# Optimization experiments

Measured on AMD Instinct MI355X. Metric: run time of the kernel, lower is better.

The kernel has to match this reference:

```python
import jax, jax.numpy as jnp
import numpy as np

N_NET, D, N_H, N_T, N_IN, N_OUT = 1, 4, 8, 2048, 256, 256


def setup_inputs() -> dict:
    key = jax.random.key(0)
    k1, k2, k3 = jax.random.split(key, 3)
    r_prime = jax.random.normal(k1, (N_NET, D, N_T, N_IN), dtype=jnp.float32)
    # learned params per __init__: E ~ N(0, 0.02), Q ~ N(0, 0.02)
    E = 0.02 * jax.random.normal(k2, (N_NET, N_H, N_OUT, N_IN), dtype=jnp.float32)
    Q = 0.02 * jax.random.normal(k3, (N_NET, N_H, N_IN, N_IN), dtype=jnp.float32)
    return {"r_prime": r_prime, "E": E, "Q": Q}


def reference(r_prime, E, Q):
    n_t = r_prime.shape[2]
    # Omega[N,b,h,t,u] = r'[N,b,t,i] Q[N,h,i,j] r'[N,b,u,j]  (bilinear scores, no softmax)
    Omega = jnp.einsum('Nbti,Nhij,Nbuj->Nbhtu', r_prime, Q, r_prime)
    mask = jnp.tril(jnp.ones((n_t, n_t), dtype=Omega.dtype))  # causal lower-triangular
    Omega = Omega * mask
    # r[N,b,t,i] = Omega[N,b,h,t,u] E[N,h,i,j] r'[N,b,u,j]
    r = jnp.einsum('Nbhtu,Nhij,Nbuj->Nbti', Omega, E, r_prime)
    return r
```

## Files before the change

kernel.cpp:

```cpp
#include <hip/hip_runtime.h>
#include <stdint.h>

typedef unsigned short u16;
typedef __attribute__((ext_vector_type(4))) float f32x4;
typedef __attribute__((ext_vector_type(4))) uint32_t u32x4;
typedef __attribute__((ext_vector_type(8))) __bf16 bf16x8;

#define B_ 4
#define H_ 8
#define T_ 2048
#define C_ 256
#define KC 2048
#define NCH 32
#define XP 528
#define SP 144

static __device__ __forceinline__ f32x4 mfma16(u32x4 a, u32x4 b, f32x4 c) {
  union { u32x4 u; bf16x8 b; } A, Bb;
  A.u = a; Bb.u = b;
  return __builtin_amdgcn_mfma_f32_16x16x32_bf16(A.b, Bb.b, c, 0, 0, 0);
}
static __device__ __forceinline__ u16 f2b(float f) {
  union { __bf16 h; u16 u; } r; r.h = (__bf16)f; return r.u;
}

__global__ __launch_bounds__(256) void k_prep(const float* __restrict__ rp_f,
                                              const float* __restrict__ E_f,
                                              const float* __restrict__ Q_f,
                                              u16* __restrict__ rbf,
                                              u16* __restrict__ rpT,
                                              u16* __restrict__ qtb,
                                              u16* __restrict__ ec) {
  __shared__ u16 l[64][72];
  const int r = blockIdx.x, tid = threadIdx.x;
  if (r < 512) {
    const int b = r >> 7, i0 = ((r >> 5) & 3) * 64, t0 = (r & 31) * 64;
    const int tj = tid & 63, tq = tid >> 6;
    const float* src = rp_f + (size_t)b * T_ * C_;
    u16* rb = rbf + (size_t)b * T_ * C_;
    #pragma unroll
    for (int rr = 0; rr < 16; ++rr) {
      int tl = rr * 4 + tq;
      u16 v = f2b(src[(size_t)(t0 + tl) * C_ + i0 + tj]);
      l[tl][tj] = v;
      rb[(size_t)(t0 + tl) * C_ + i0 + tj] = v;
    }
    __syncthreads();
    u16* dst = rpT + (size_t)b * C_ * T_;
    #pragma unroll
    for (int rr = 0; rr < 16; ++rr) {
      int il = rr * 4 + tq;
      dst[(size_t)(i0 + il) * T_ + t0 + tj] = l[tj][il];
    }
  } else if (r < 640) {
    const int q = r - 512;
    const int h = q >> 4, i0 = ((q >> 2) & 3) * 64, j0 = (q & 3) * 64;
    const int tj = tid & 63, tq = tid >> 6;
    const float* qh = Q_f + (size_t)h * C_ * C_;
    #pragma unroll
    for (int rr = 0; rr < 16; ++rr) {
      int i = rr * 4 + tq;
      l[i][tj] = f2b(qh[(size_t)(i0 + i) * C_ + j0 + tj]);
    }
    __syncthreads();
    u16* qth = qtb + (size_t)h * C_ * C_;
    #pragma unroll
    for (int rr = 0; rr < 16; ++rr) {
      int j = rr * 4 + tq;
      qth[(size_t)(j0 + j) * C_ + i0 + tj] = l[tj][j];
    }
  } else {
    const int q = r - 640;
    size_t e = ((size_t)q * 256 + tid) * 4;
    int h = (int)(e >> 16), i = (int)((e >> 8) & 255), j = (int)(e & 255);
    f32x4 v = *(const f32x4*)(E_f + e);
    union { u16 h4[4]; uint64_t qq; } p;
    #pragma unroll
    for (int c = 0; c < 4; ++c) p.h4[c] = f2b(v[c]);
    *(uint64_t*)(ec + (size_t)i * KC + h * 256 + j) = p.qq;
  }
}

__global__ __launch_bounds__(256) void k_gram(const u16* __restrict__ rpT,
                                              u16* __restrict__ G) {
  __shared__ u16 gls[4][16][20];
  const int js = blockIdx.x, iq = blockIdx.y, b = blockIdx.z;
  const int tid = threadIdx.x, lane = tid & 63, v = tid >> 6;
  const int l15 = lane & 15, lq = lane >> 4;
  const u16* rtb = rpT + (size_t)b * C_ * T_;
  const int irow = 64 * iq + 16 * v;
  const int rrow = lane >> 2, rc4 = (lane & 3) * 4;

  f32x4 acc = (f32x4)0.f;

  for (int k = 0; k < NCH; ++k) {
    #pragma unroll
    for (int rr = 0; rr < 4; ++rr)
      gls[v][4 * lq + rr][l15] = f2b(acc[rr]);
    __builtin_amdgcn_wave_barrier();
    u16* gk = G + (size_t)(b * NCH + k) * C_ * C_;
    *(uint64_t*)(gk + (size_t)(irow + rrow) * C_ + 16 * js + rc4) =
        *(const uint64_t*)&gls[v][rrow][rc4];
    __builtin_amdgcn_wave_barrier();

    u32x4 am[2], bn[2];
    #pragma unroll
    for (int kk = 0; kk < 2; ++kk) {
      am[kk] = *(const u32x4*)(rtb + (size_t)(irow + l15) * T_ +
                               64 * k + 32 * kk + 8 * lq);
      bn[kk] = *(const u32x4*)(rtb + (size_t)(16 * js + l15) * T_ +
                               64 * k + 32 * kk + 8 * lq);
    }
    #pragma unroll
    for (int kk = 0; kk < 2; ++kk)
      acc = mfma16(am[kk], bn[kk], acc);
  }
}

__global__ __launch_bounds__(256, 2) void k_z(const u16* __restrict__ rbf,
                                              const u16* __restrict__ rpT,
                                              const u16* __restrict__ qtb,
                                              const u16* __restrict__ G,
                                              u16* __restrict__ ZC) {
  __shared__ __align__(16) char rp_l[64 * XP];
  __shared__ __align__(16) char x_l[64 * XP];
  __shared__ __align__(16) char s_l[64 * SP];

  const int tile = blockIdx.x, b = blockIdx.y, h = blockIdx.z;
  const int t0 = tile * 64;
  const int tid = threadIdx.x, lane = tid & 63, v = tid >> 6;
  const int l15 = lane & 15, lq = lane >> 4;

  const u16* rpb = rbf + (size_t)b * T_ * C_;
  const u16* rtb = rpT + (size_t)b * C_ * T_;
  const u16* gt  = G + (size_t)(b * NCH + tile) * C_ * C_;
  const u16* qth = qtb + (size_t)h * C_ * C_;

  {
    const int row = tid >> 2, seg = tid & 3;
    const char* src = (const char*)(rpb + (size_t)(t0 + row) * C_);
    #pragma unroll
    for (int c = 0; c < 8; ++c) {
      u32x4 vv = *(const u32x4*)(src + seg * 128 + c * 16);
      *(u32x4*)(rp_l + (size_t)row * XP + seg * 128 + c * 16) = vv;
    }
  }
  __syncthreads();

  #pragma unroll
  for (int mh = 0; mh < 2; ++mh) {
    u32x4 am[2][8];
    #pragma unroll
    for (int mq = 0; mq < 2; ++mq)
      #pragma unroll
      for (int kk = 0; kk < 8; ++kk)
        am[mq][kk] = *(const u32x4*)(rp_l +
            (size_t)(32 * mh + 16 * mq + l15) * XP + 64 * kk + 16 * lq);
    #pragma unroll
    for (int n = 0; n < 4; ++n) {
      f32x4 qacc[2];
      qacc[0] = (f32x4)0.f; qacc[1] = (f32x4)0.f;
      #pragma unroll
      for (int kk = 0; kk < 8; ++kk) {
        u32x4 bq = *(const u32x4*)(qth +
            (size_t)(64 * v + 16 * n + l15) * C_ + 32 * kk + 8 * lq);
        qacc[0] = mfma16(am[0][kk], bq, qacc[0]);
        qacc[1] = mfma16(am[1][kk], bq, qacc[1]);
      }
      #pragma unroll
      for (int mq = 0; mq < 2; ++mq)
        #pragma unroll
        for (int rr = 0; rr < 4; ++rr)
          *(u16*)(x_l + (size_t)(32 * mh + 16 * mq + 4 * lq + rr) * XP +
                  (64 * v + 16 * n + l15) * 2) = f2b(qacc[mq][rr]);
    }
  }
  __syncthreads();

  f32x4 acc[4][4];
  #pragma unroll
  for (int m = 0; m < 4; ++m)
    #pragma unroll
    for (int n = 0; n < 4; ++n) acc[m][n] = (f32x4)0.f;

  #pragma unroll
  for (int n = 0; n < 4; ++n) {
    u32x4 bg[8];
    #pragma unroll
    for (int kk = 0; kk < 8; ++kk)
      bg[kk] = *(const u32x4*)(gt +
          (size_t)(64 * v + 16 * n + l15) * C_ + 32 * kk + 8 * lq);
    #pragma unroll
    for (int mm = 0; mm < 4; ++mm) {
      u32x4 qa2[8];
      #pragma unroll
      for (int kk = 0; kk < 8; ++kk)
        qa2[kk] = *(const u32x4*)(x_l + (size_t)(16 * mm + l15) * XP +
                                  64 * kk + 16 * lq);
      #pragma unroll
      for (int kk = 0; kk < 8; ++kk)
        acc[mm][n] = mfma16(qa2[kk], bg[kk], acc[mm][n]);
    }
  }

  {
    f32x4 sacc[4];
    #pragma unroll
    for (int m = 0; m < 4; ++m) sacc[m] = (f32x4)0.f;
    u32x4 bs[8];
    #pragma unroll
    for (int kk = 0; kk < 8; ++kk)
      bs[kk] = *(const u32x4*)(rp_l + (size_t)(16 * v + l15) * XP +
                               64 * kk + 16 * lq);
    #pragma unroll
    for (int mm = 0; mm < 4; ++mm) {
      u32x4 qa2[8];
      #pragma unroll
      for (int kk = 0; kk < 8; ++kk)
        qa2[kk] = *(const u32x4*)(x_l + (size_t)(16 * mm + l15) * XP +
                                  64 * kk + 16 * lq);
      #pragma unroll
      for (int kk = 0; kk < 8; ++kk)
        sacc[mm] = mfma16(qa2[kk], bs[kk], sacc[mm]);
    }
    #pragma unroll
    for (int m = 0; m < 4; ++m)
      #pragma unroll
      for (int rr = 0; rr < 4; ++rr) {
        int tl = 16 * m + 4 * lq + rr;
        int ul = 16 * v + l15;
        float sv = (ul > tl) ? 0.f : sacc[m][rr];
        *(u16*)(s_l + (size_t)tl * SP + ul * 2) = f2b(sv);
      }
  }
  __syncthreads();

  {
    u32x4 sa[4][2];
    #pragma unroll
    for (int m = 0; m < 4; ++m)
      #pragma unroll
      for (int kk = 0; kk < 2; ++kk)
        sa[m][kk] = *(const u32x4*)(s_l + (size_t)(16 * m + l15) * SP +
                                    64 * kk + 16 * lq);
    #pragma unroll
    for (int n = 0; n < 4; ++n)
      #pragma unroll
      for (int kk = 0; kk < 2; ++kk) {
        u32x4 vb = *(const u32x4*)(rtb +
            (size_t)(64 * v + 16 * n + l15) * T_ + t0 + 32 * kk + 8 * lq);
        #pragma unroll
        for (int m = 0; m < 4; ++m)
          acc[m][n] = mfma16(sa[m][kk], vb, acc[m][n]);
      }
  }

  #pragma unroll
  for (int m = 0; m < 4; ++m)
    #pragma unroll
    for (int n = 0; n < 4; ++n)
      #pragma unroll
      for (int rr = 0; rr < 4; ++rr)
        *(u16*)(x_l + (size_t)(16 * m + 4 * lq + rr) * XP +
                (64 * v + 16 * n + l15) * 2) = f2b(acc[m][n][rr]);
  __syncthreads();
  {
    const int row = tid >> 2, seg = tid & 3;
    char* dst = (char*)(ZC + ((size_t)(b * T_ + t0 + row) * KC + h * 256));
    #pragma unroll
    for (int c = 0; c < 8; ++c) {
      u32x4 vv = *(const u32x4*)(x_l + (size_t)row * XP + seg * 128 + c * 16);
      *(u32x4*)(dst + seg * 128 + c * 16) = vv;
    }
  }
}

__global__ __launch_bounds__(256) void k_o(const u16* __restrict__ ZC,
                                           const u16* __restrict__ ec,
                                           float* __restrict__ out) {
  const int mt = blockIdx.x, b = blockIdx.y;
  const int tid = threadIdx.x, lane = tid & 63, v = tid >> 6;
  const int l15 = lane & 15, lq = lane >> 4;

  const u16* za_b = ZC + (size_t)(b * T_ + mt * 32) * KC;

  f32x4 acc[2][4];
  #pragma unroll
  for (int m = 0; m < 2; ++m)
    #pragma unroll
    for (int n = 0; n < 4; ++n) acc[m][n] = (f32x4)0.f;

  #pragma unroll 2
  for (int kk = 0; kk < 64; ++kk) {
    u32x4 am[2], bn[4];
    #pragma unroll
    for (int m = 0; m < 2; ++m)
      am[m] = *(const u32x4*)(za_b + (size_t)(16 * m + l15) * KC +
                              32 * kk + 8 * lq);
    #pragma unroll
    for (int n = 0; n < 4; ++n)
      bn[n] = *(const u32x4*)(ec + (size_t)(64 * v + 16 * n + l15) * KC +
                              32 * kk + 8 * lq);
    #pragma unroll
    for (int m = 0; m < 2; ++m)
      #pragma unroll
      for (int n = 0; n < 4; ++n)
        acc[m][n] = mfma16(am[m], bn[n], acc[m][n]);
  }

  float* ob = out + ((size_t)b * T_ + mt * 32) * C_;
  #pragma unroll
  for (int m = 0; m < 2; ++m)
    #pragma unroll
    for (int n = 0; n < 4; ++n)
      #pragma unroll
      for (int rr = 0; rr < 4; ++rr)
        ob[(size_t)(16 * m + 4 * lq + rr) * C_ + 64 * v + 16 * n + l15] =
            acc[m][n][rr];
}

extern "C" void kernel_launch(void* const* d_in, const int* in_sizes, int n_in,
                              void* d_out, int out_size, void* d_ws, size_t ws_size,
                              hipStream_t stream) {
  (void)ws_size; (void)out_size;
  const float* rp_f = nullptr;
  const float* sm[2] = {nullptr, nullptr};
  int ns = 0;
  for (int i = 0; i < n_in; ++i) {
    if (in_sizes[i] == 2097152) {
      rp_f = (const float*)d_in[i];
    } else if (ns < 2) {
      sm[ns++] = (const float*)d_in[i];
    }
  }
  const float* E_f = sm[0];
  const float* Q_f = sm[1];

  const size_t MB = 1024 * 1024;
  u16* G   = (u16*)d_ws;
  u16* rbf = (u16*)((char*)d_ws + 16 * MB);
  u16* rpT = (u16*)((char*)d_ws + 20 * MB);
  u16* qtb = (u16*)((char*)d_ws + 24 * MB);
  u16* ec  = (u16*)((char*)d_ws + 25 * MB);
  u16* ZC  = (u16*)((char*)d_ws + 26 * MB);
  float* outf = (float*)d_out;

  k_prep<<<1152, 256, 0, stream>>>(rp_f, E_f, Q_f, rbf, rpT, qtb, ec);
  k_gram<<<dim3(16, 4, 4), 256, 0, stream>>>(rpT, G);
  k_z<<<dim3(32, 4, 8), 256, 0, stream>>>(rbf, rpT, qtb, G, ZC);
  k_o<<<dim3(64, 4), 256, 0, stream>>>(ZC, ec, outf);
}
```

Measured before the change: 142.9 us.

## Halve k_z tile rows to 32 to double grid and drop rp LDS staging

The k_z kernel now processes 32 query rows per block instead of 64, doubling the grid to 2048 blocks so more blocks run across the CUs. The r' tile is read straight from global memory rather than staged in shared memory. The intra-chunk score block is recomputed over the enclosing 64-row chunk, with a global causal mask, and the prefix Gram matrix is indexed by the 64-chunk. This cuts LDS use and raises occupancy, at the cost of recomputing the Q projection and re-reading G and r' in two blocks per chunk.

New measurement: 176.5 us. 23.5% more time.

```diff
diff --git a/kernel.cpp b/kernel.cpp
--- a/kernel.cpp
+++ b/kernel.cpp
@@ -117,45 +117,34 @@
   }
 }
 
-__global__ __launch_bounds__(256, 2) void k_z(const u16* __restrict__ rbf,
-                                              const u16* __restrict__ rpT,
-                                              const u16* __restrict__ qtb,
-                                              const u16* __restrict__ G,
-                                              u16* __restrict__ ZC) {
-  __shared__ __align__(16) char rp_l[64 * XP];
-  __shared__ __align__(16) char x_l[64 * XP];
-  __shared__ __align__(16) char s_l[64 * SP];
-
-  const int tile = blockIdx.x, b = blockIdx.y, h = blockIdx.z;
-  const int t0 = tile * 64;
+__global__ __launch_bounds__(256) void k_z(const u16* __restrict__ rbf,
+                                           const u16* __restrict__ rpT,
+                                           const u16* __restrict__ qtb,
+                                           const u16* __restrict__ G,
+                                           u16* __restrict__ ZC) {
+  __shared__ __align__(16) char x_l[32 * XP];
+  __shared__ __align__(16) char s_l[32 * SP];
+
+  const int tt = blockIdx.x, b = blockIdx.y, h = blockIdx.z;
+  const int t0 = tt * 32;
+  const int u0 = t0 & ~63;
+  const int kch = tt >> 1;
   const int tid = threadIdx.x, lane = tid & 63, v = tid >> 6;
   const int l15 = lane & 15, lq = lane >> 4;
 
   const u16* rpb = rbf + (size_t)b * T_ * C_;
   const u16* rtb = rpT + (size_t)b * C_ * T_;
-  const u16* gt  = G + (size_t)(b * NCH + tile) * C_ * C_;
+  const u16* gt  = G + (size_t)(b * NCH + kch) * C_ * C_;
   const u16* qth = qtb + (size_t)h * C_ * C_;
 
   {
-    const int row = tid >> 2, seg = tid & 3;
-    const char* src = (const char*)(rpb + (size_t)(t0 + row) * C_);
-    #pragma unroll
-    for (int c = 0; c < 8; ++c) {
-      u32x4 vv = *(const u32x4*)(src + seg * 128 + c * 16);
-      *(u32x4*)(rp_l + (size_t)row * XP + seg * 128 + c * 16) = vv;
-    }
-  }
-  __syncthreads();
-
-  #pragma unroll
-  for (int mh = 0; mh < 2; ++mh) {
     u32x4 am[2][8];
     #pragma unroll
     for (int mq = 0; mq < 2; ++mq)
       #pragma unroll
       for (int kk = 0; kk < 8; ++kk)
-        am[mq][kk] = *(const u32x4*)(rp_l +
-            (size_t)(32 * mh + 16 * mq + l15) * XP + 64 * kk + 16 * lq);
+        am[mq][kk] = *(const u32x4*)(rpb +
+            (size_t)(t0 + 16 * mq + l15) * C_ + 32 * kk + 8 * lq);
     #pragma unroll
     for (int n = 0; n < 4; ++n) {
       f32x4 qacc[2];
@@ -171,15 +160,15 @@
       for (int mq = 0; mq < 2; ++mq)
         #pragma unroll
         for (int rr = 0; rr < 4; ++rr)
-          *(u16*)(x_l + (size_t)(32 * mh + 16 * mq + 4 * lq + rr) * XP +
+          *(u16*)(x_l + (size_t)(16 * mq + 4 * lq + rr) * XP +
                   (64 * v + 16 * n + l15) * 2) = f2b(qacc[mq][rr]);
     }
   }
   __syncthreads();
 
-  f32x4 acc[4][4];
-  #pragma unroll
-  for (int m = 0; m < 4; ++m)
+  f32x4 acc[2][4];
+  #pragma unroll
+  for (int m = 0; m < 2; ++m)
     #pragma unroll
     for (int n = 0; n < 4; ++n) acc[m][n] = (f32x4)0.f;
 
@@ -191,7 +180,7 @@
       bg[kk] = *(const u32x4*)(gt +
           (size_t)(64 * v + 16 * n + l15) * C_ + 32 * kk + 8 * lq);
     #pragma unroll
-    for (int mm = 0; mm < 4; ++mm) {
+    for (int mm = 0; mm < 2; ++mm) {
       u32x4 qa2[8];
       #pragma unroll
       for (int kk = 0; kk < 8; ++kk)
@@ -204,41 +193,37 @@
   }
 
   {
-    f32x4 sacc[4];
-    #pragma unroll
-    for (int m = 0; m < 4; ++m) sacc[m] = (f32x4)0.f;
-    u32x4 bs[8];
+    const int sr = v >> 1, sc = v & 1;
+    u32x4 qa3[8];
     #pragma unroll
     for (int kk = 0; kk < 8; ++kk)
-      bs[kk] = *(const u32x4*)(rp_l + (size_t)(16 * v + l15) * XP +
-                               64 * kk + 16 * lq);
-    #pragma unroll
-    for (int mm = 0; mm < 4; ++mm) {
-      u32x4 qa2[8];
-      #pragma unroll
-      for (int kk = 0; kk < 8; ++kk)
-        qa2[kk] = *(const u32x4*)(x_l + (size_t)(16 * mm + l15) * XP +
-                                  64 * kk + 16 * lq);
-      #pragma unroll
-      for (int kk = 0; kk < 8; ++kk)
-        sacc[mm] = mfma16(qa2[kk], bs[kk], sacc[mm]);
-    }
-    #pragma unroll
-    for (int m = 0; m < 4; ++m)
+      qa3[kk] = *(const u32x4*)(x_l + (size_t)(16 * sr + l15) * XP +
+                                64 * kk + 16 * lq);
+    #pragma unroll
+    for (int n2 = 0; n2 < 2; ++n2) {
+      f32x4 sacc = (f32x4)0.f;
+      #pragma unroll
+      for (int kk = 0; kk < 8; ++kk) {
+        u32x4 bs = *(const u32x4*)(rpb +
+            (size_t)(u0 + 32 * sc + 16 * n2 + l15) * C_ + 32 * kk + 8 * lq);
+        sacc = mfma16(qa3[kk], bs, sacc);
+      }
       #pragma unroll
       for (int rr = 0; rr < 4; ++rr) {
-        int tl = 16 * m + 4 * lq + rr;
-        int ul = 16 * v + l15;
-        float sv = (ul > tl) ? 0.f : sacc[m][rr];
-        *(u16*)(s_l + (size_t)tl * SP + ul * 2) = f2b(sv);
+        int tg = t0 + 16 * sr + 4 * lq + rr;
+        int ug = u0 + 32 * sc + 16 * n2 + l15;
+        float sv = (ug > tg) ? 0.f : sacc[rr];
+        *(u16*)(s_l + (size_t)(16 * sr + 4 * lq + rr) * SP +
+                (32 * sc + 16 * n2 + l15) * 2) = f2b(sv);
       }
+    }
   }
   __syncthreads();
 
   {
-    u32x4 sa[4][2];
-    #pragma unroll
-    for (int m = 0; m < 4; ++m)
+    u32x4 sa[2][2];
+    #pragma unroll
+    for (int m = 0; m < 2; ++m)
       #pragma unroll
       for (int kk = 0; kk < 2; ++kk)
         sa[m][kk] = *(const u32x4*)(s_l + (size_t)(16 * m + l15) * SP +
@@ -248,15 +233,15 @@
       #pragma unroll
       for (int kk = 0; kk < 2; ++kk) {
         u32x4 vb = *(const u32x4*)(rtb +
-            (size_t)(64 * v + 16 * n + l15) * T_ + t0 + 32 * kk + 8 * lq);
+            (size_t)(64 * v + 16 * n + l15) * T_ + u0 + 32 * kk + 8 * lq);
         #pragma unroll
-        for (int m = 0; m < 4; ++m)
+        for (int m = 0; m < 2; ++m)
           acc[m][n] = mfma16(sa[m][kk], vb, acc[m][n]);
       }
   }
 
   #pragma unroll
-  for (int m = 0; m < 4; ++m)
+  for (int m = 0; m < 2; ++m)
     #pragma unroll
     for (int n = 0; n < 4; ++n)
       #pragma unroll
@@ -265,12 +250,12 @@
                 (64 * v + 16 * n + l15) * 2) = f2b(acc[m][n][rr]);
   __syncthreads();
   {
-    const int row = tid >> 2, seg = tid & 3;
+    const int row = tid >> 3, seg = tid & 7;
     char* dst = (char*)(ZC + ((size_t)(b * T_ + t0 + row) * KC + h * 256));
     #pragma unroll
-    for (int c = 0; c < 8; ++c) {
-      u32x4 vv = *(const u32x4*)(x_l + (size_t)row * XP + seg * 128 + c * 16);
-      *(u32x4*)(dst + seg * 128 + c * 16) = vv;
+    for (int c = 0; c < 4; ++c) {
+      u32x4 vv = *(const u32x4*)(x_l + (size_t)row * XP + seg * 64 + c * 16);
+      *(u32x4*)(dst + seg * 64 + c * 16) = vv;
     }
   }
 }
@@ -347,6 +332,6 @@
 
   k_prep<<<1152, 256, 0, stream>>>(rp_f, E_f, Q_f, rbf, rpT, qtb, ec);
   k_gram<<<dim3(16, 4, 4), 256, 0, stream>>>(rpT, G);
-  k_z<<<dim3(32, 4, 8), 256, 0, stream>>>(rbf, rpT, qtb, G, ZC);
+  k_z<<<dim3(64, 4, 8), 256, 0, stream>>>(rbf, rpT, qtb, G, ZC);
   k_o<<<dim3(64, 4), 256, 0, stream>>>(ZC, ec, outf);
 }
```
